# Kernel optimization log

Hardware: AMD Instinct MI355X
Metric: run time of the kernel (lower is better)

## Reference

```python
import jax, jax.numpy as jnp
import numpy as np

B, N, L, D, DP, H = 1, 128, 256, 256, 128, 8
DH = D // H
LN_EPS = 1e-5


def setup_inputs() -> dict:
    key = jax.random.key(0)
    ks = jax.random.split(key, 8)
    w = lambda k, shape: jax.random.normal(k, shape, jnp.float32) * 0.02
    return {
        "msa": jax.random.normal(ks[0], (B, N, L, D), jnp.float32),
        "pair_bias": jax.random.normal(ks[1], (B, L, L, DP), jnp.float32),
        "msa_mask": jnp.ones((B, N, L), jnp.int32),
        "ln_g": jnp.ones((D,), jnp.float32),
        "ln_b": jnp.zeros((D,), jnp.float32),
        "Wq": w(ks[2], (D, D)), "bq": jnp.zeros((D,), jnp.float32),
        "Wk": w(ks[3], (D, D)), "bk": jnp.zeros((D,), jnp.float32),
        "Wv": w(ks[4], (D, D)), "bv": jnp.zeros((D,), jnp.float32),
        "Wb": w(ks[5], (DP, H)), "bb": jnp.zeros((H,), jnp.float32),
        "Wo": w(ks[6], (D, D)), "bo": jnp.zeros((D,), jnp.float32),
        # gate initialized as in the torch module: zero weight, ones bias
        "Wg": jnp.zeros((D, D), jnp.float32), "bg": jnp.ones((D,), jnp.float32),
    }


def reference(msa, pair_bias, msa_mask, ln_g, ln_b, Wq, bq, Wk, bk, Wv, bv,
              Wb, bb, Wo, bo, Wg, bg):
    b, n, l, d = msa.shape
    h = bb.shape[0]
    dh = d // h
    # LayerNorm over d_msa
    mu = msa.mean(-1, keepdims=True)
    var = msa.var(-1, keepdims=True)
    xn = (msa - mu) * jax.lax.rsqrt(var + LN_EPS) * ln_g + ln_b
    # projections -> [b, n, l, h, dh]
    q = (xn @ Wq + bq).reshape(b, n, l, h, dh)
    k = (xn @ Wk + bk).reshape(b, n, l, h, dh)
    v = (xn @ Wv + bv).reshape(b, n, l, h, dh)
    scores = jnp.einsum('bnihd,bnjhd->bnhij', q, k) / jnp.sqrt(jnp.float32(dh))
    # pair bias: [b, l, l, h] -> [b, 1, h, l, l], broadcast over N_seq
    bias = (pair_bias @ Wb + bb).transpose(0, 3, 1, 2)[:, None]
    scores = scores + bias
    # mask over key axis
    mask = msa_mask[:, :, None, None, :].astype(bool)
    scores = jnp.where(mask, scores, jnp.float32(-1e9))
    attn = jax.nn.softmax(scores, axis=-1)  # dropout is identity at eval
    out = jnp.einsum('bnhij,bnjhd->bnihd', attn, v).reshape(b, n, l, d)
    out = out @ Wo + bo
    gate = jax.nn.sigmoid(xn @ Wg + bg)
    return out * gate
```

## Files before the change

kernel.cpp:

```cpp
#include <hip/hip_runtime.h>
#include <hip/hip_bf16.h>

typedef __attribute__((ext_vector_type(4))) float f32x4;
typedef __attribute__((ext_vector_type(16))) float f32x16;
typedef __attribute__((ext_vector_type(8))) __bf16 bf16x8;
typedef __attribute__((ext_vector_type(4))) __bf16 bf16x4;
typedef __attribute__((ext_vector_type(2))) __bf16 bf16x2;
typedef __attribute__((ext_vector_type(4))) unsigned u32x4;
typedef __attribute__((ext_vector_type(2))) unsigned u32x2;

#define VTS 264
#define L2E 1.4426950408889634f

#define GLOAD_LDS16(g, l) __builtin_amdgcn_global_load_lds( \
    (const __attribute__((address_space(1))) void*)(g),     \
    (__attribute__((address_space(3))) void*)(l), 16, 0, 0)

#if __has_builtin(__builtin_amdgcn_permlane32_swap)
#define SWP(a, b) { u32x2 _r = __builtin_amdgcn_permlane32_swap((a), (b), false, false); \
                    (a) = _r[0]; (b) = _r[1]; }
#else
#define SWP(a, b) { unsigned _sa = __shfl_xor((a), 32), _sb = __shfl_xor((b), 32); \
                    unsigned _na = hi ? _sb : (a); (b) = hi ? (b) : _sa; (a) = _na; }
#endif
#define SUM32(ts, lrun) { (lrun) += (ts) + __shfl_xor((ts), 32); }

__global__ __launch_bounds__(256) void ln_kernel(
    const float* __restrict__ msa, const float* __restrict__ g,
    const float* __restrict__ b, __bf16* __restrict__ xn)
{
  const int row = blockIdx.x * 4 + (threadIdx.x >> 6);
  const int lane = threadIdx.x & 63;
  const float* src = msa + (size_t)row * 256 + lane * 4;
  f32x4 x = *(const f32x4*)src;
  float s = x[0] + x[1] + x[2] + x[3];
  float s2 = x[0]*x[0] + x[1]*x[1] + x[2]*x[2] + x[3]*x[3];
#pragma unroll
  for (int d = 32; d >= 1; d >>= 1) {
    s  += __shfl_xor(s, d);
    s2 += __shfl_xor(s2, d);
  }
  const float mu  = s * (1.f / 256.f);
  const float inv = rsqrtf(s2 * (1.f / 256.f) - mu * mu + 1e-5f);
  const f32x4 gv = *(const f32x4*)(g + lane * 4);
  const f32x4 bv = *(const f32x4*)(b + lane * 4);
  bf16x4 o;
#pragma unroll
  for (int j = 0; j < 4; ++j) o[j] = (__bf16)((x[j] - mu) * inv * gv[j] + bv[j]);
  *(bf16x4*)(xn + (size_t)row * 256 + lane * 4) = o;
}

__global__ __launch_bounds__(256) void bias_kernel(
    const float* __restrict__ pair, const float* __restrict__ Wb,
    const float* __restrict__ bb, float* __restrict__ biasf)
{
  __shared__ float wbs[1024];
  const int t = threadIdx.x;
#pragma unroll
  for (int r2 = 0; r2 < 4; ++r2) wbs[t + 256 * r2] = Wb[t + 256 * r2];
  __syncthreads();
  const int i = blockIdx.x, j = t;
  const float* src = pair + ((size_t)i * 256 + j) * 128;
  float acc[8];
#pragma unroll
  for (int hh = 0; hh < 8; ++hh) acc[hh] = bb[hh];
  for (int p = 0; p < 128; p += 4) {
    const f32x4 pv = *(const f32x4*)(src + p);
#pragma unroll
    for (int q2 = 0; q2 < 4; ++q2)
#pragma unroll
      for (int hh = 0; hh < 8; ++hh) acc[hh] += pv[q2] * wbs[(p + q2) * 8 + hh];
  }
#pragma unroll
  for (int hh = 0; hh < 8; ++hh)
    biasf[((size_t)hh * 256 + i) * 256 + j] = acc[hh] * L2E;
}

__global__ __launch_bounds__(256) void prep_kernel(
    const float* __restrict__ Wq, const float* __restrict__ Wk,
    const float* __restrict__ Wv, const float* __restrict__ Wg,
    const float* __restrict__ Wo, __bf16* __restrict__ Wt)
{
  const int w = blockIdx.x >> 8, n2 = blockIdx.x & 255, k = threadIdx.x;
  const float* W = (w == 0) ? Wq : (w == 1) ? Wk : (w == 2) ? Wv : (w == 3) ? Wg : Wo;
  Wt[((size_t)w * 256 + n2) * 256 + k] = (__bf16)W[(size_t)k * 256 + n2];
}

__global__ __launch_bounds__(256) void qkvg_gemm(
    const __bf16* __restrict__ xn, const __bf16* __restrict__ Wt,
    const float* __restrict__ bq, const float* __restrict__ bk,
    const float* __restrict__ bv, const float* __restrict__ bg,
    __bf16* __restrict__ qb, __bf16* __restrict__ kb,
    __bf16* __restrict__ vb, __bf16* __restrict__ gateb)
{
  __shared__ alignas(16) __bf16 Al[128 * 64];
  __shared__ alignas(16) __bf16 Bl[128 * 64];
  const int t = threadIdx.x;
  const int wave = t >> 6, lane = t & 63;
  const int l15 = lane & 15, l16 = lane >> 4;
  const int bid = blockIdx.x;
  const int xcd = bid & 7, idx = bid >> 3;
  const int m0 = (xcd * 32 + (idx & 31)) * 128;
  const int bn = idx >> 5;
  const int w = bn >> 1;
  const int nloc0 = (bn & 1) * 128;
  const __bf16* Wtw = Wt + (size_t)w * 65536;
  const int wm = (wave >> 1) * 64, wn = (wave & 1) * 64;

  const int srow = (lane >> 3);
  const int chunk = ((lane & 7) ^ srow) * 8;

  f32x4 acc[4][4];
#pragma unroll
  for (int i = 0; i < 4; ++i)
#pragma unroll
    for (int j = 0; j < 4; ++j) acc[i][j] = (f32x4){0.f, 0.f, 0.f, 0.f};

  for (int kt = 0; kt < 4; ++kt) {
    const int k0 = kt * 64;
#pragma unroll
    for (int i = 0; i < 4; ++i) {
      const int row = wave * 32 + i * 8 + srow;
      GLOAD_LDS16(xn  + (size_t)(m0 + row) * 256 + k0 + chunk,  &Al[(wave * 4 + i) * 512]);
      GLOAD_LDS16(Wtw + (size_t)(nloc0 + row) * 256 + k0 + chunk, &Bl[(wave * 4 + i) * 512]);
    }
    __syncthreads();
#pragma unroll
    for (int kk = 0; kk < 2; ++kk) {
      bf16x8 a[4], bfr[4];
#pragma unroll
      for (int mi = 0; mi < 4; ++mi) {
        const int row = wm + mi * 16 + l15;
        a[mi] = *(const bf16x8*)&Al[row * 64 + ((kk * 32 + l16 * 8) ^ ((row & 7) << 3))];
      }
#pragma unroll
      for (int ni = 0; ni < 4; ++ni) {
        const int row = wn + ni * 16 + l15;
        bfr[ni] = *(const bf16x8*)&Bl[row * 64 + ((kk * 32 + l16 * 8) ^ ((row & 7) << 3))];
      }
#pragma unroll
      for (int mi = 0; mi < 4; ++mi)
#pragma unroll
        for (int ni = 0; ni < 4; ++ni)
          acc[mi][ni] = __builtin_amdgcn_mfma_f32_16x16x32_bf16(a[mi], bfr[ni], acc[mi][ni], 0, 0, 0);
    }
    __syncthreads();
  }

  const float* bias_arr = (w == 0) ? bq : (w == 1) ? bk : (w == 2) ? bv : bg;
  float bnis[4];
#pragma unroll
  for (int ni = 0; ni < 4; ++ni) bnis[ni] = bias_arr[nloc0 + wn + ni * 16 + l15];
  const float qscale = 0.17677669529663687f * L2E;

#pragma unroll
  for (int mi = 0; mi < 4; ++mi)
#pragma unroll
    for (int ni = 0; ni < 4; ++ni)
#pragma unroll
      for (int r = 0; r < 4; ++r) {
        const int grow = m0 + wm + mi * 16 + l16 * 4 + r;
        const int gcol = nloc0 + wn + ni * 16 + l15;
        const float v = acc[mi][ni][r] + bnis[ni];
        const int n = grow >> 8, i2 = grow & 255, h = gcol >> 5, dh = gcol & 31;
        const size_t hoff = (((size_t)n * 8 + h) * 256 + i2) * 32 + dh;
        if (w == 0)      qb[hoff] = (__bf16)(v * qscale);
        else if (w == 1) kb[hoff] = (__bf16)v;
        else if (w == 2) vb[hoff] = (__bf16)v;
        else gateb[(size_t)grow * 256 + gcol] = (__bf16)(1.f / (1.f + __expf(-v)));
      }
}

__device__ __forceinline__ unsigned pk2(float a, float b) {
  bf16x2 t; t[0] = (__bf16)a; t[1] = (__bf16)b;
  return __builtin_bit_cast(unsigned, t);
}

__global__ __launch_bounds__(256) void attn_kernel(
    const __bf16* __restrict__ qb, const __bf16* __restrict__ kb,
    const __bf16* __restrict__ vb, const float* __restrict__ biasf,
    const int* __restrict__ mask, __bf16* __restrict__ opre)
{
  __shared__ alignas(16) __bf16 Vt[32 * VTS];
  __shared__ alignas(16) float Ml[256];
  const int t = threadIdx.x, wave = t >> 6, lane = t & 63;
  const int l31 = lane & 31, hi = lane >> 5;
  const int bid = blockIdx.x, nh = bid >> 1, half = bid & 1;
  const int n = nh >> 3, h = nh & 7;
  const __bf16* kbh = kb + (size_t)nh * 8192;
  const __bf16* qbh = qb + (size_t)nh * 8192;

  {
    const bf16x8* vs = (const bf16x8*)(vb + (size_t)nh * 8192 + t * 32);
    bf16x8 vv[4];
#pragma unroll
    for (int j = 0; j < 4; ++j) vv[j] = vs[j];
#pragma unroll
    for (int j = 0; j < 4; ++j)
#pragma unroll
      for (int e = 0; e < 8; ++e) Vt[(j * 8 + e) * VTS + t] = vv[j][e];
    Ml[t] = mask[n * 256 + t] ? 0.f : -1e9f;
  }
  __syncthreads();

  const int q0 = half * 128 + wave * 32;
  const int q = q0 + l31;
  const bf16x8 Qf0 = *(const bf16x8*)(qbh + (size_t)q * 32 + hi * 8);
  const bf16x8 Qf1 = *(const bf16x8*)(qbh + (size_t)q * 32 + 16 + hi * 8);

  const float* bp = biasf + (size_t)h * 65536 + (size_t)q * 256;

  bf16x8 Kc0 = *(const bf16x8*)(kbh + (size_t)l31 * 32 + hi * 8);
  bf16x8 Kc1 = *(const bf16x8*)(kbh + (size_t)l31 * 32 + 16 + hi * 8);
  f32x4 bc[4];
#pragma unroll
  for (int g = 0; g < 4; ++g) {
    const f32x4 bv = *(const f32x4*)(bp + 8 * g + 4 * hi);
    const f32x4 mk = *(const f32x4*)&Ml[8 * g + 4 * hi];
    bc[g] = bv + mk;
  }

  f32x16 Ot;
#pragma unroll
  for (int r = 0; r < 16; ++r) Ot[r] = 0.f;
  float lrun = 0.f;

#pragma unroll 2
  for (int kt = 0; kt < 8; ++kt) {
    const int k0 = kt * 32;
    const int ktn = (kt + 1) & 7;
    f32x16 st;
#pragma unroll
    for (int g = 0; g < 4; ++g)
#pragma unroll
      for (int e = 0; e < 4; ++e) st[4 * g + e] = bc[g][e];
    st = __builtin_amdgcn_mfma_f32_32x32x16_bf16(Kc0, Qf0, st, 0, 0, 0);
    st = __builtin_amdgcn_mfma_f32_32x32x16_bf16(Kc1, Qf1, st, 0, 0, 0);
    Kc0 = *(const bf16x8*)(kbh + (size_t)(ktn * 32 + l31) * 32 + hi * 8);
    Kc1 = *(const bf16x8*)(kbh + (size_t)(ktn * 32 + l31) * 32 + 16 + hi * 8);
#pragma unroll
    for (int g = 0; g < 4; ++g) {
      const f32x4 bv = *(const f32x4*)(bp + ktn * 32 + 8 * g + 4 * hi);
      const f32x4 mk = *(const f32x4*)&Ml[ktn * 32 + 8 * g + 4 * hi];
      bc[g] = bv + mk;
    }
#pragma unroll
    for (int r = 0; r < 16; ++r) st[r] = exp2f(st[r]);
    float ts = st[0];
#pragma unroll
    for (int r = 1; r < 16; ++r) ts += st[r];
    SUM32(ts, lrun);
    unsigned c0 = pk2(st[0],  st[1]),  c1 = pk2(st[2],  st[3]);
    unsigned c2 = pk2(st[4],  st[5]),  c3 = pk2(st[6],  st[7]);
    unsigned c4 = pk2(st[8],  st[9]),  c5 = pk2(st[10], st[11]);
    unsigned c6 = pk2(st[12], st[13]), c7 = pk2(st[14], st[15]);
    SWP(c0, c2); SWP(c1, c3); SWP(c4, c6); SWP(c5, c7);
    u32x4 w0 = {c0, c1, c2, c3}, w1 = {c4, c5, c6, c7};
    const bf16x8 pf0 = __builtin_bit_cast(bf16x8, w0);
    const bf16x8 pf1 = __builtin_bit_cast(bf16x8, w1);
    const bf16x8 Vf0 = *(const bf16x8*)&Vt[l31 * VTS + k0 + hi * 8];
    const bf16x8 Vf1 = *(const bf16x8*)&Vt[l31 * VTS + k0 + 16 + hi * 8];
    Ot = __builtin_amdgcn_mfma_f32_32x32x16_bf16(Vf0, pf0, Ot, 0, 0, 0);
    Ot = __builtin_amdgcn_mfma_f32_32x32x16_bf16(Vf1, pf1, Ot, 0, 0, 0);
  }

  const float invl = 1.f / lrun;
  unsigned P00 = pk2(Ot[0]  * invl, Ot[1]  * invl), P01 = pk2(Ot[2]  * invl, Ot[3]  * invl);
  unsigned P10 = pk2(Ot[4]  * invl, Ot[5]  * invl), P11 = pk2(Ot[6]  * invl, Ot[7]  * invl);
  unsigned P20 = pk2(Ot[8]  * invl, Ot[9]  * invl), P21 = pk2(Ot[10] * invl, Ot[11] * invl);
  unsigned P30 = pk2(Ot[12] * invl, Ot[13] * invl), P31 = pk2(Ot[14] * invl, Ot[15] * invl);
  SWP(P00, P20); SWP(P01, P21); SWP(P10, P30); SWP(P11, P31);
  u32x4 s0 = {P00, P01, P20, P21}, s1 = {P10, P11, P30, P31};
  __bf16* dst = opre + (((size_t)h * 128 + n) * 256 + q) * 32 + hi * 16;
  *(u32x4*)dst = s0;
  *(u32x4*)(dst + 8) = s1;
}

__global__ __launch_bounds__(256) void wo_gemm(
    const __bf16* __restrict__ A, const __bf16* __restrict__ Wtw,
    const float* __restrict__ bo, const __bf16* __restrict__ gateb,
    float* __restrict__ out)
{
  __shared__ alignas(16) __bf16 Al[128 * 64];
  __shared__ alignas(16) __bf16 Bl[128 * 64];
  const int t = threadIdx.x;
  const int wave = t >> 6, lane = t & 63;
  const int l15 = lane & 15, l16 = lane >> 4;
  const int bid = blockIdx.x;
  const int xcd = bid & 7, idx = bid >> 3;
  const int m0 = (xcd * 32 + (idx & 31)) * 128;
  const int nloc0 = (idx >> 5) * 128;
  const int wm = (wave >> 1) * 64, wn = (wave & 1) * 64;

  const int srow = (lane >> 3);
  const int chunk = ((lane & 7) ^ srow) * 8;

  f32x4 acc[4][4];
#pragma unroll
  for (int i = 0; i < 4; ++i)
#pragma unroll
    for (int j = 0; j < 4; ++j) acc[i][j] = (f32x4){0.f, 0.f, 0.f, 0.f};

  for (int kt = 0; kt < 4; ++kt) {
    const int k0 = kt * 64;
#pragma unroll
    for (int i = 0; i < 4; ++i) {
      const int row = wave * 32 + i * 8 + srow;
      const int m = m0 + row;
      const int kg = k0 + chunk;
      GLOAD_LDS16(A + (size_t)(kg >> 5) * 1048576 + (size_t)(m >> 8) * 8192
                    + (m & 255) * 32 + (kg & 31),
                  &Al[(wave * 4 + i) * 512]);
      GLOAD_LDS16(Wtw + (size_t)(nloc0 + row) * 256 + kg, &Bl[(wave * 4 + i) * 512]);
    }
    __syncthreads();
#pragma unroll
    for (int kk = 0; kk < 2; ++kk) {
      bf16x8 a[4], bfr[4];
#pragma unroll
      for (int mi = 0; mi < 4; ++mi) {
        const int row = wm + mi * 16 + l15;
        a[mi] = *(const bf16x8*)&Al[row * 64 + ((kk * 32 + l16 * 8) ^ ((row & 7) << 3))];
      }
#pragma unroll
      for (int ni = 0; ni < 4; ++ni) {
        const int row = wn + ni * 16 + l15;
        bfr[ni] = *(const bf16x8*)&Bl[row * 64 + ((kk * 32 + l16 * 8) ^ ((row & 7) << 3))];
      }
#pragma unroll
      for (int mi = 0; mi < 4; ++mi)
#pragma unroll
        for (int ni = 0; ni < 4; ++ni)
          acc[mi][ni] = __builtin_amdgcn_mfma_f32_16x16x32_bf16(a[mi], bfr[ni], acc[mi][ni], 0, 0, 0);
    }
    __syncthreads();
  }

  float bov[4];
#pragma unroll
  for (int ni = 0; ni < 4; ++ni) bov[ni] = bo[nloc0 + wn + ni * 16 + l15];
#pragma unroll
  for (int mi = 0; mi < 4; ++mi)
#pragma unroll
    for (int ni = 0; ni < 4; ++ni)
#pragma unroll
      for (int r = 0; r < 4; ++r) {
        const int grow = m0 + wm + mi * 16 + l16 * 4 + r;
        const int gcol = nloc0 + wn + ni * 16 + l15;
        const size_t o = (size_t)grow * 256 + gcol;
        out[o] = (acc[mi][ni][r] + bov[ni]) * (float)gateb[o];
      }
}

extern "C" void kernel_launch(void* const* d_in, const int* in_sizes, int n_in,
                              void* d_out, int out_size, void* d_ws, size_t ws_size,
                              hipStream_t stream)
{
  const float* msa  = (const float*)d_in[0];
  const float* pair = (const float*)d_in[1];
  const int*   mask = (const int*)d_in[2];
  const float* ln_g = (const float*)d_in[3];
  const float* ln_b = (const float*)d_in[4];
  const float* Wq = (const float*)d_in[5];  const float* bq = (const float*)d_in[6];
  const float* Wk = (const float*)d_in[7];  const float* bk = (const float*)d_in[8];
  const float* Wv = (const float*)d_in[9];  const float* bv = (const float*)d_in[10];
  const float* Wb = (const float*)d_in[11]; const float* bb = (const float*)d_in[12];
  const float* Wo = (const float*)d_in[13]; const float* bo = (const float*)d_in[14];
  const float* Wg = (const float*)d_in[15]; const float* bg = (const float*)d_in[16];
  float* out = (float*)d_out;

  char* ws = (char*)d_ws;
  __bf16* xn    = (__bf16*)(ws);
  __bf16* qb    = (__bf16*)(ws + 16777216);
  __bf16* kb    = (__bf16*)(ws + 2 * 16777216);
  __bf16* vb    = (__bf16*)(ws + 3 * 16777216);
  __bf16* opre  = (__bf16*)(ws + 4 * 16777216);
  __bf16* Wt    = (__bf16*)(ws + 5 * 16777216);
  __bf16* gateb = (__bf16*)(ws + 5 * 16777216 + 655360);
  float*  biasf = (float*)(ws + 5 * 16777216 + 655360 + 16777216);

  hipLaunchKernelGGL(ln_kernel,   dim3(8192), dim3(256), 0, stream, msa, ln_g, ln_b, xn);
  hipLaunchKernelGGL(bias_kernel, dim3(256),  dim3(256), 0, stream, pair, Wb, bb, biasf);
  hipLaunchKernelGGL(prep_kernel, dim3(1280), dim3(256), 0, stream, Wq, Wk, Wv, Wg, Wo, Wt);
  hipLaunchKernelGGL(qkvg_gemm,   dim3(2048), dim3(256), 0, stream, xn, Wt, bq, bk, bv, bg, qb, kb, vb, gateb);
  hipLaunchKernelGGL(attn_kernel, dim3(2048), dim3(256), 0, stream, qb, kb, vb, biasf, mask, opre);
  hipLaunchKernelGGL(wo_gemm,     dim3(512),  dim3(256), 0, stream, opre, Wt + 4 * 65536, bo, gateb, out);
}
```

Measured before the change: 138.9 us.

## Fuse setup kernels, stage GEMM epilogue through LDS, restructure attention bias/mask loads

Merges the layernorm, pair-bias projection and weight transpose kernels into one launch, with block-index ranges selecting the work, to remove two kernel launches and their gaps. The QKVG GEMM epilogue now writes bf16 results into the reused LDS tiles and then emits 16-byte row-contiguous global stores, replacing scattered 2-byte stores. In attention, the mask add moves next to its use and the loop unroll drops to 1, which lowers register pressure at the cost of less overlap between iterations. Sharing one setup kernel forces LDS allocation on the layernorm blocks too, which may lower their occupancy.

```diff
diff --git a/kernel.cpp b/kernel.cpp
--- a/kernel.cpp
+++ b/kernel.cpp
@@ -25,65 +25,62 @@
 #endif
 #define SUM32(ts, lrun) { (lrun) += (ts) + __shfl_xor((ts), 32); }
 
-__global__ __launch_bounds__(256) void ln_kernel(
+__global__ __launch_bounds__(256) void setup_kernel(
     const float* __restrict__ msa, const float* __restrict__ g,
-    const float* __restrict__ b, __bf16* __restrict__ xn)
-{
-  const int row = blockIdx.x * 4 + (threadIdx.x >> 6);
-  const int lane = threadIdx.x & 63;
-  const float* src = msa + (size_t)row * 256 + lane * 4;
-  f32x4 x = *(const f32x4*)src;
-  float s = x[0] + x[1] + x[2] + x[3];
-  float s2 = x[0]*x[0] + x[1]*x[1] + x[2]*x[2] + x[3]*x[3];
-#pragma unroll
-  for (int d = 32; d >= 1; d >>= 1) {
-    s  += __shfl_xor(s, d);
-    s2 += __shfl_xor(s2, d);
-  }
-  const float mu  = s * (1.f / 256.f);
-  const float inv = rsqrtf(s2 * (1.f / 256.f) - mu * mu + 1e-5f);
-  const f32x4 gv = *(const f32x4*)(g + lane * 4);
-  const f32x4 bv = *(const f32x4*)(b + lane * 4);
-  bf16x4 o;
-#pragma unroll
-  for (int j = 0; j < 4; ++j) o[j] = (__bf16)((x[j] - mu) * inv * gv[j] + bv[j]);
-  *(bf16x4*)(xn + (size_t)row * 256 + lane * 4) = o;
-}
-
-__global__ __launch_bounds__(256) void bias_kernel(
+    const float* __restrict__ b, __bf16* __restrict__ xn,
     const float* __restrict__ pair, const float* __restrict__ Wb,
-    const float* __restrict__ bb, float* __restrict__ biasf)
-{
-  __shared__ float wbs[1024];
-  const int t = threadIdx.x;
-#pragma unroll
-  for (int r2 = 0; r2 < 4; ++r2) wbs[t + 256 * r2] = Wb[t + 256 * r2];
-  __syncthreads();
-  const int i = blockIdx.x, j = t;
-  const float* src = pair + ((size_t)i * 256 + j) * 128;
-  float acc[8];
-#pragma unroll
-  for (int hh = 0; hh < 8; ++hh) acc[hh] = bb[hh];
-  for (int p = 0; p < 128; p += 4) {
-    const f32x4 pv = *(const f32x4*)(src + p);
-#pragma unroll
-    for (int q2 = 0; q2 < 4; ++q2)
-#pragma unroll
-      for (int hh = 0; hh < 8; ++hh) acc[hh] += pv[q2] * wbs[(p + q2) * 8 + hh];
-  }
-#pragma unroll
-  for (int hh = 0; hh < 8; ++hh)
-    biasf[((size_t)hh * 256 + i) * 256 + j] = acc[hh] * L2E;
-}
-
-__global__ __launch_bounds__(256) void prep_kernel(
+    const float* __restrict__ bb, float* __restrict__ biasf,
     const float* __restrict__ Wq, const float* __restrict__ Wk,
     const float* __restrict__ Wv, const float* __restrict__ Wg,
     const float* __restrict__ Wo, __bf16* __restrict__ Wt)
 {
-  const int w = blockIdx.x >> 8, n2 = blockIdx.x & 255, k = threadIdx.x;
-  const float* W = (w == 0) ? Wq : (w == 1) ? Wk : (w == 2) ? Wv : (w == 3) ? Wg : Wo;
-  Wt[((size_t)w * 256 + n2) * 256 + k] = (__bf16)W[(size_t)k * 256 + n2];
+  __shared__ float wbs[1024];
+  const int bid = blockIdx.x;
+  const int t = threadIdx.x;
+  if (bid < 8192) {
+    const int row = bid * 4 + (t >> 6);
+    const int lane = t & 63;
+    f32x4 x = *(const f32x4*)(msa + (size_t)row * 256 + lane * 4);
+    float s = x[0] + x[1] + x[2] + x[3];
+    float s2 = x[0]*x[0] + x[1]*x[1] + x[2]*x[2] + x[3]*x[3];
+#pragma unroll
+    for (int d = 32; d >= 1; d >>= 1) {
+      s  += __shfl_xor(s, d);
+      s2 += __shfl_xor(s2, d);
+    }
+    const float mu  = s * (1.f / 256.f);
+    const float inv = rsqrtf(s2 * (1.f / 256.f) - mu * mu + 1e-5f);
+    const f32x4 gv = *(const f32x4*)(g + lane * 4);
+    const f32x4 bv = *(const f32x4*)(b + lane * 4);
+    bf16x4 o;
+#pragma unroll
+    for (int j = 0; j < 4; ++j) o[j] = (__bf16)((x[j] - mu) * inv * gv[j] + bv[j]);
+    *(bf16x4*)(xn + (size_t)row * 256 + lane * 4) = o;
+  } else if (bid < 8448) {
+#pragma unroll
+    for (int r2 = 0; r2 < 4; ++r2) wbs[t + 256 * r2] = Wb[t + 256 * r2];
+    __syncthreads();
+    const int i = bid - 8192, j = t;
+    const float* src = pair + ((size_t)i * 256 + j) * 128;
+    float acc[8];
+#pragma unroll
+    for (int hh = 0; hh < 8; ++hh) acc[hh] = bb[hh];
+    for (int p = 0; p < 128; p += 4) {
+      const f32x4 pv = *(const f32x4*)(src + p);
+#pragma unroll
+      for (int q2 = 0; q2 < 4; ++q2)
+#pragma unroll
+        for (int hh = 0; hh < 8; ++hh) acc[hh] += pv[q2] * wbs[(p + q2) * 8 + hh];
+    }
+#pragma unroll
+    for (int hh = 0; hh < 8; ++hh)
+      biasf[((size_t)hh * 256 + i) * 256 + j] = acc[hh] * L2E;
+  } else {
+    const int idx = bid - 8448;
+    const int w = idx >> 8, n2 = idx & 255, k = t;
+    const float* W = (w == 0) ? Wq : (w == 1) ? Wk : (w == 2) ? Wv : (w == 3) ? Wg : Wo;
+    Wt[((size_t)w * 256 + n2) * 256 + k] = (__bf16)W[(size_t)k * 256 + n2];
+  }
 }
 
 __global__ __launch_bounds__(256) void qkvg_gemm(
@@ -153,22 +150,42 @@
   for (int ni = 0; ni < 4; ++ni) bnis[ni] = bias_arr[nloc0 + wn + ni * 16 + l15];
   const float qscale = 0.17677669529663687f * L2E;
 
-#pragma unroll
-  for (int mi = 0; mi < 4; ++mi)
-#pragma unroll
-    for (int ni = 0; ni < 4; ++ni)
-#pragma unroll
-      for (int r = 0; r < 4; ++r) {
-        const int grow = m0 + wm + mi * 16 + l16 * 4 + r;
-        const int gcol = nloc0 + wn + ni * 16 + l15;
-        const float v = acc[mi][ni][r] + bnis[ni];
-        const int n = grow >> 8, i2 = grow & 255, h = gcol >> 5, dh = gcol & 31;
-        const size_t hoff = (((size_t)n * 8 + h) * 256 + i2) * 32 + dh;
-        if (w == 0)      qb[hoff] = (__bf16)(v * qscale);
-        else if (w == 1) kb[hoff] = (__bf16)v;
-        else if (w == 2) vb[hoff] = (__bf16)v;
-        else gateb[(size_t)grow * 256 + gcol] = (__bf16)(1.f / (1.f + __expf(-v)));
-      }
+  __bf16* Tw = ((wave < 2) ? Al : Bl) + (wave & 1) * (32 * 72);
+  const int lrow = lane >> 1, lcol = (lane & 1) * 32;
+  __bf16* db2 = (w == 0) ? qb : (w == 1) ? kb : vb;
+#pragma unroll
+  for (int half = 0; half < 2; ++half) {
+#pragma unroll
+    for (int m2 = 0; m2 < 2; ++m2) {
+      const int mi = half * 2 + m2;
+#pragma unroll
+      for (int ni = 0; ni < 4; ++ni)
+#pragma unroll
+        for (int r = 0; r < 4; ++r) {
+          const float v = acc[mi][ni][r] + bnis[ni];
+          __bf16 val;
+          if (w == 0)      val = (__bf16)(v * qscale);
+          else if (w == 3) val = (__bf16)(1.f / (1.f + __expf(-v)));
+          else             val = (__bf16)v;
+          Tw[(m2 * 16 + l16 * 4 + r) * 72 + ni * 16 + l15] = val;
+        }
+    }
+    bf16x8 rowv[4];
+#pragma unroll
+    for (int c = 0; c < 4; ++c) rowv[c] = *(const bf16x8*)&Tw[lrow * 72 + lcol + c * 8];
+    const int grow = m0 + wm + half * 32 + lrow;
+    const int n = grow >> 8, i2 = grow & 255;
+    if (w < 3) {
+      const int hA = (nloc0 + wn + lcol) >> 5;
+      __bf16* dst = db2 + (((size_t)n * 8 + hA) * 256 + i2) * 32;
+#pragma unroll
+      for (int c = 0; c < 4; ++c) *(bf16x8*)(dst + c * 8) = rowv[c];
+    } else {
+      __bf16* dst = gateb + (size_t)grow * 256 + nloc0 + wn + lcol;
+#pragma unroll
+      for (int c = 0; c < 4; ++c) *(bf16x8*)(dst + c * 8) = rowv[c];
+    }
+  }
 }
 
 __device__ __forceinline__ unsigned pk2(float a, float b) {
@@ -214,36 +231,31 @@
   bf16x8 Kc1 = *(const bf16x8*)(kbh + (size_t)l31 * 32 + 16 + hi * 8);
   f32x4 bc[4];
 #pragma unroll
-  for (int g = 0; g < 4; ++g) {
-    const f32x4 bv = *(const f32x4*)(bp + 8 * g + 4 * hi);
-    const f32x4 mk = *(const f32x4*)&Ml[8 * g + 4 * hi];
-    bc[g] = bv + mk;
-  }
+  for (int g = 0; g < 4; ++g) bc[g] = *(const f32x4*)(bp + 8 * g + 4 * hi);
 
   f32x16 Ot;
 #pragma unroll
   for (int r = 0; r < 16; ++r) Ot[r] = 0.f;
   float lrun = 0.f;
 
-#pragma unroll 2
+#pragma unroll 1
   for (int kt = 0; kt < 8; ++kt) {
     const int k0 = kt * 32;
     const int ktn = (kt + 1) & 7;
     f32x16 st;
 #pragma unroll
-    for (int g = 0; g < 4; ++g)
-#pragma unroll
-      for (int e = 0; e < 4; ++e) st[4 * g + e] = bc[g][e];
+    for (int g = 0; g < 4; ++g) {
+      const f32x4 mk = *(const f32x4*)&Ml[k0 + 8 * g + 4 * hi];
+#pragma unroll
+      for (int e = 0; e < 4; ++e) st[4 * g + e] = bc[g][e] + mk[e];
+    }
     st = __builtin_amdgcn_mfma_f32_32x32x16_bf16(Kc0, Qf0, st, 0, 0, 0);
     st = __builtin_amdgcn_mfma_f32_32x32x16_bf16(Kc1, Qf1, st, 0, 0, 0);
     Kc0 = *(const bf16x8*)(kbh + (size_t)(ktn * 32 + l31) * 32 + hi * 8);
     Kc1 = *(const bf16x8*)(kbh + (size_t)(ktn * 32 + l31) * 32 + 16 + hi * 8);
 #pragma unroll
-    for (int g = 0; g < 4; ++g) {
-      const f32x4 bv = *(const f32x4*)(bp + ktn * 32 + 8 * g + 4 * hi);
-      const f32x4 mk = *(const f32x4*)&Ml[ktn * 32 + 8 * g + 4 * hi];
-      bc[g] = bv + mk;
-    }
+    for (int g = 0; g < 4; ++g)
+      bc[g] = *(const f32x4*)(bp + ktn * 32 + 8 * g + 4 * hi);
 #pragma unroll
     for (int r = 0; r < 16; ++r) st[r] = exp2f(st[r]);
     float ts = st[0];
@@ -379,9 +391,8 @@
   __bf16* gateb = (__bf16*)(ws + 5 * 16777216 + 655360);
   float*  biasf = (float*)(ws + 5 * 16777216 + 655360 + 16777216);
 
-  hipLaunchKernelGGL(ln_kernel,   dim3(8192), dim3(256), 0, stream, msa, ln_g, ln_b, xn);
-  hipLaunchKernelGGL(bias_kernel, dim3(256),  dim3(256), 0, stream, pair, Wb, bb, biasf);
-  hipLaunchKernelGGL(prep_kernel, dim3(1280), dim3(256), 0, stream, Wq, Wk, Wv, Wg, Wo, Wt);
+  hipLaunchKernelGGL(setup_kernel, dim3(9728), dim3(256), 0, stream,
+                     msa, ln_g, ln_b, xn, pair, Wb, bb, biasf, Wq, Wk, Wv, Wg, Wo, Wt);
   hipLaunchKernelGGL(qkvg_gemm,   dim3(2048), dim3(256), 0, stream, xn, Wt, bq, bk, bv, bg, qb, kb, vb, gateb);
   hipLaunchKernelGGL(attn_kernel, dim3(2048), dim3(256), 0, stream, qb, kb, vb, biasf, mask, opre);
   hipLaunchKernelGGL(wo_gemm,     dim3(512),  dim3(256), 0, stream, opre, Wt + 4 * 65536, bo, gateb, out);
```

Result: no change. 140.1 us (+0.8%).

## Merge setup kernels into one launch and stage K tiles in LDS for attention

Applied to the files above, without the earlier changes.

The layernorm, pair-bias projection and weight-transpose kernels are combined into a single launch that branches on block index. This removes two launches and the idle gaps between them, and lets the independent setup work overlap. The attention kernel now copies the whole per-head K tile into padded shared memory once and reads K fragments from LDS, instead of prefetching them from global memory inside the loop. That costs about 20 KB more LDS per block, which may lower occupancy, and the loop unroll factor drops from 2 to 1.

```diff
diff --git a/kernel.cpp b/kernel.cpp
--- a/kernel.cpp
+++ b/kernel.cpp
@@ -10,6 +10,7 @@
 typedef __attribute__((ext_vector_type(2))) unsigned u32x2;
 
 #define VTS 264
+#define KLS 40
 #define L2E 1.4426950408889634f
 
 #define GLOAD_LDS16(g, l) __builtin_amdgcn_global_load_lds( \
@@ -25,65 +26,62 @@
 #endif
 #define SUM32(ts, lrun) { (lrun) += (ts) + __shfl_xor((ts), 32); }
 
-__global__ __launch_bounds__(256) void ln_kernel(
+__global__ __launch_bounds__(256) void setup_kernel(
     const float* __restrict__ msa, const float* __restrict__ g,
-    const float* __restrict__ b, __bf16* __restrict__ xn)
-{
-  const int row = blockIdx.x * 4 + (threadIdx.x >> 6);
-  const int lane = threadIdx.x & 63;
-  const float* src = msa + (size_t)row * 256 + lane * 4;
-  f32x4 x = *(const f32x4*)src;
-  float s = x[0] + x[1] + x[2] + x[3];
-  float s2 = x[0]*x[0] + x[1]*x[1] + x[2]*x[2] + x[3]*x[3];
-#pragma unroll
-  for (int d = 32; d >= 1; d >>= 1) {
-    s  += __shfl_xor(s, d);
-    s2 += __shfl_xor(s2, d);
-  }
-  const float mu  = s * (1.f / 256.f);
-  const float inv = rsqrtf(s2 * (1.f / 256.f) - mu * mu + 1e-5f);
-  const f32x4 gv = *(const f32x4*)(g + lane * 4);
-  const f32x4 bv = *(const f32x4*)(b + lane * 4);
-  bf16x4 o;
-#pragma unroll
-  for (int j = 0; j < 4; ++j) o[j] = (__bf16)((x[j] - mu) * inv * gv[j] + bv[j]);
-  *(bf16x4*)(xn + (size_t)row * 256 + lane * 4) = o;
-}
-
-__global__ __launch_bounds__(256) void bias_kernel(
+    const float* __restrict__ b, __bf16* __restrict__ xn,
     const float* __restrict__ pair, const float* __restrict__ Wb,
-    const float* __restrict__ bb, float* __restrict__ biasf)
-{
-  __shared__ float wbs[1024];
-  const int t = threadIdx.x;
-#pragma unroll
-  for (int r2 = 0; r2 < 4; ++r2) wbs[t + 256 * r2] = Wb[t + 256 * r2];
-  __syncthreads();
-  const int i = blockIdx.x, j = t;
-  const float* src = pair + ((size_t)i * 256 + j) * 128;
-  float acc[8];
-#pragma unroll
-  for (int hh = 0; hh < 8; ++hh) acc[hh] = bb[hh];
-  for (int p = 0; p < 128; p += 4) {
-    const f32x4 pv = *(const f32x4*)(src + p);
-#pragma unroll
-    for (int q2 = 0; q2 < 4; ++q2)
-#pragma unroll
-      for (int hh = 0; hh < 8; ++hh) acc[hh] += pv[q2] * wbs[(p + q2) * 8 + hh];
-  }
-#pragma unroll
-  for (int hh = 0; hh < 8; ++hh)
-    biasf[((size_t)hh * 256 + i) * 256 + j] = acc[hh] * L2E;
-}
-
-__global__ __launch_bounds__(256) void prep_kernel(
+    const float* __restrict__ bb, float* __restrict__ biasf,
     const float* __restrict__ Wq, const float* __restrict__ Wk,
     const float* __restrict__ Wv, const float* __restrict__ Wg,
     const float* __restrict__ Wo, __bf16* __restrict__ Wt)
 {
-  const int w = blockIdx.x >> 8, n2 = blockIdx.x & 255, k = threadIdx.x;
-  const float* W = (w == 0) ? Wq : (w == 1) ? Wk : (w == 2) ? Wv : (w == 3) ? Wg : Wo;
-  Wt[((size_t)w * 256 + n2) * 256 + k] = (__bf16)W[(size_t)k * 256 + n2];
+  __shared__ float wbs[1024];
+  const int bid = blockIdx.x;
+  const int t = threadIdx.x;
+  if (bid < 8192) {
+    const int row = bid * 4 + (t >> 6);
+    const int lane = t & 63;
+    f32x4 x = *(const f32x4*)(msa + (size_t)row * 256 + lane * 4);
+    float s = x[0] + x[1] + x[2] + x[3];
+    float s2 = x[0]*x[0] + x[1]*x[1] + x[2]*x[2] + x[3]*x[3];
+#pragma unroll
+    for (int d = 32; d >= 1; d >>= 1) {
+      s  += __shfl_xor(s, d);
+      s2 += __shfl_xor(s2, d);
+    }
+    const float mu  = s * (1.f / 256.f);
+    const float inv = rsqrtf(s2 * (1.f / 256.f) - mu * mu + 1e-5f);
+    const f32x4 gv = *(const f32x4*)(g + lane * 4);
+    const f32x4 bv = *(const f32x4*)(b + lane * 4);
+    bf16x4 o;
+#pragma unroll
+    for (int j = 0; j < 4; ++j) o[j] = (__bf16)((x[j] - mu) * inv * gv[j] + bv[j]);
+    *(bf16x4*)(xn + (size_t)row * 256 + lane * 4) = o;
+  } else if (bid < 8448) {
+#pragma unroll
+    for (int r2 = 0; r2 < 4; ++r2) wbs[t + 256 * r2] = Wb[t + 256 * r2];
+    __syncthreads();
+    const int i = bid - 8192, j = t;
+    const float* src = pair + ((size_t)i * 256 + j) * 128;
+    float acc[8];
+#pragma unroll
+    for (int hh = 0; hh < 8; ++hh) acc[hh] = bb[hh];
+    for (int p = 0; p < 128; p += 4) {
+      const f32x4 pv = *(const f32x4*)(src + p);
+#pragma unroll
+      for (int q2 = 0; q2 < 4; ++q2)
+#pragma unroll
+        for (int hh = 0; hh < 8; ++hh) acc[hh] += pv[q2] * wbs[(p + q2) * 8 + hh];
+    }
+#pragma unroll
+    for (int hh = 0; hh < 8; ++hh)
+      biasf[((size_t)hh * 256 + i) * 256 + j] = acc[hh] * L2E;
+  } else {
+    const int idx = bid - 8448;
+    const int w = idx >> 8, n2 = idx & 255, k = t;
+    const float* W = (w == 0) ? Wq : (w == 1) ? Wk : (w == 2) ? Wv : (w == 3) ? Wg : Wo;
+    Wt[((size_t)w * 256 + n2) * 256 + k] = (__bf16)W[(size_t)k * 256 + n2];
+  }
 }
 
 __global__ __launch_bounds__(256) void qkvg_gemm(
@@ -181,16 +179,22 @@
     const __bf16* __restrict__ vb, const float* __restrict__ biasf,
     const int* __restrict__ mask, __bf16* __restrict__ opre)
 {
+  __shared__ alignas(16) __bf16 Kl[256 * KLS];
   __shared__ alignas(16) __bf16 Vt[32 * VTS];
   __shared__ alignas(16) float Ml[256];
   const int t = threadIdx.x, wave = t >> 6, lane = t & 63;
   const int l31 = lane & 31, hi = lane >> 5;
   const int bid = blockIdx.x, nh = bid >> 1, half = bid & 1;
   const int n = nh >> 3, h = nh & 7;
-  const __bf16* kbh = kb + (size_t)nh * 8192;
   const __bf16* qbh = qb + (size_t)nh * 8192;
 
   {
+    const bf16x8* ks = (const bf16x8*)(kb + (size_t)nh * 8192 + t * 32);
+    bf16x8 kr[4];
+#pragma unroll
+    for (int j = 0; j < 4; ++j) kr[j] = ks[j];
+#pragma unroll
+    for (int j = 0; j < 4; ++j) *(bf16x8*)&Kl[t * KLS + j * 8] = kr[j];
     const bf16x8* vs = (const bf16x8*)(vb + (size_t)nh * 8192 + t * 32);
     bf16x8 vv[4];
 #pragma unroll
@@ -210,8 +214,6 @@
 
   const float* bp = biasf + (size_t)h * 65536 + (size_t)q * 256;
 
-  bf16x8 Kc0 = *(const bf16x8*)(kbh + (size_t)l31 * 32 + hi * 8);
-  bf16x8 Kc1 = *(const bf16x8*)(kbh + (size_t)l31 * 32 + 16 + hi * 8);
   f32x4 bc[4];
 #pragma unroll
   for (int g = 0; g < 4; ++g) {
@@ -225,19 +227,21 @@
   for (int r = 0; r < 16; ++r) Ot[r] = 0.f;
   float lrun = 0.f;
 
-#pragma unroll 2
+#pragma unroll 1
   for (int kt = 0; kt < 8; ++kt) {
     const int k0 = kt * 32;
     const int ktn = (kt + 1) & 7;
+    const bf16x8 Kf0 = *(const bf16x8*)&Kl[(k0 + l31) * KLS + hi * 8];
+    const bf16x8 Kf1 = *(const bf16x8*)&Kl[(k0 + l31) * KLS + 16 + hi * 8];
+    const bf16x8 Vf0 = *(const bf16x8*)&Vt[l31 * VTS + k0 + hi * 8];
+    const bf16x8 Vf1 = *(const bf16x8*)&Vt[l31 * VTS + k0 + 16 + hi * 8];
     f32x16 st;
 #pragma unroll
     for (int g = 0; g < 4; ++g)
 #pragma unroll
       for (int e = 0; e < 4; ++e) st[4 * g + e] = bc[g][e];
-    st = __builtin_amdgcn_mfma_f32_32x32x16_bf16(Kc0, Qf0, st, 0, 0, 0);
-    st = __builtin_amdgcn_mfma_f32_32x32x16_bf16(Kc1, Qf1, st, 0, 0, 0);
-    Kc0 = *(const bf16x8*)(kbh + (size_t)(ktn * 32 + l31) * 32 + hi * 8);
-    Kc1 = *(const bf16x8*)(kbh + (size_t)(ktn * 32 + l31) * 32 + 16 + hi * 8);
+    st = __builtin_amdgcn_mfma_f32_32x32x16_bf16(Kf0, Qf0, st, 0, 0, 0);
+    st = __builtin_amdgcn_mfma_f32_32x32x16_bf16(Kf1, Qf1, st, 0, 0, 0);
 #pragma unroll
     for (int g = 0; g < 4; ++g) {
       const f32x4 bv = *(const f32x4*)(bp + ktn * 32 + 8 * g + 4 * hi);
@@ -258,8 +262,6 @@
     u32x4 w0 = {c0, c1, c2, c3}, w1 = {c4, c5, c6, c7};
     const bf16x8 pf0 = __builtin_bit_cast(bf16x8, w0);
     const bf16x8 pf1 = __builtin_bit_cast(bf16x8, w1);
-    const bf16x8 Vf0 = *(const bf16x8*)&Vt[l31 * VTS + k0 + hi * 8];
-    const bf16x8 Vf1 = *(const bf16x8*)&Vt[l31 * VTS + k0 + 16 + hi * 8];
     Ot = __builtin_amdgcn_mfma_f32_32x32x16_bf16(Vf0, pf0, Ot, 0, 0, 0);
     Ot = __builtin_amdgcn_mfma_f32_32x32x16_bf16(Vf1, pf1, Ot, 0, 0, 0);
   }
@@ -379,9 +381,8 @@
   __bf16* gateb = (__bf16*)(ws + 5 * 16777216 + 655360);
   float*  biasf = (float*)(ws + 5 * 16777216 + 655360 + 16777216);
 
-  hipLaunchKernelGGL(ln_kernel,   dim3(8192), dim3(256), 0, stream, msa, ln_g, ln_b, xn);
-  hipLaunchKernelGGL(bias_kernel, dim3(256),  dim3(256), 0, stream, pair, Wb, bb, biasf);
-  hipLaunchKernelGGL(prep_kernel, dim3(1280), dim3(256), 0, stream, Wq, Wk, Wv, Wg, Wo, Wt);
+  hipLaunchKernelGGL(setup_kernel, dim3(9728), dim3(256), 0, stream,
+                     msa, ln_g, ln_b, xn, pair, Wb, bb, biasf, Wq, Wk, Wv, Wg, Wo, Wt);
   hipLaunchKernelGGL(qkvg_gemm,   dim3(2048), dim3(256), 0, stream, xn, Wt, bq, bk, bv, bg, qb, kb, vb, gateb);
   hipLaunchKernelGGL(attn_kernel, dim3(2048), dim3(256), 0, stream, qb, kb, vb, biasf, mask, opre);
   hipLaunchKernelGGL(wo_gemm,     dim3(512),  dim3(256), 0, stream, opre, Wt + 4 * 65536, bo, gateb, out);
```

After: 134.5 us. 3.2% less time.
